# Kernel optimization log

Measured on AMD Instinct MI355X. Metric: run time of the kernel, lower is better.

Reference implementation:

```python
import jax, jax.numpy as jnp
import numpy as np

IN_SIZE = 256
HIDDEN = 512
T = 32768


def setup_inputs() -> dict:
    key = jax.random.key(0)
    ks = jax.random.split(key, 6)
    lim_ih = 1.0 / np.sqrt(HIDDEN)
    inp = {
        "input": jax.random.normal(ks[0], (T, IN_SIZE), dtype=jnp.float32),
        "init_hidden": jax.random.normal(ks[1], (HIDDEN,), dtype=jnp.float32),
        # eqx.nn.GRUCell parameters: weight_ih (3H, in), weight_hh (3H, H), bias (3H,), bias_n (H,)
        "weight_ih": jax.random.uniform(ks[2], (3 * HIDDEN, IN_SIZE), minval=-lim_ih, maxval=lim_ih, dtype=jnp.float32),
        "weight_hh": jax.random.uniform(ks[3], (3 * HIDDEN, HIDDEN), minval=-lim_ih, maxval=lim_ih, dtype=jnp.float32),
        "bias": jax.random.uniform(ks[4], (3 * HIDDEN,), minval=-lim_ih, maxval=lim_ih, dtype=jnp.float32),
        "bias_n": jax.random.uniform(ks[5], (HIDDEN,), minval=-lim_ih, maxval=lim_ih, dtype=jnp.float32),
    }
    return inp


def reference(input, init_hidden, weight_ih, weight_hh, bias, bias_n):
    H = init_hidden.shape[0]
    # Precompute all input-side gates in one big GEMM: [T, 3H]
    igates_all = input @ weight_ih.T + bias

    def step(h, ig):
        hg = weight_hh @ h  # [3H]
        ir, iz, inn = ig[:H], ig[H:2 * H], ig[2 * H:]
        hr, hz, hn = hg[:H], hg[H:2 * H], hg[2 * H:]
        reset = jax.nn.sigmoid(ir + hr)
        upd = jax.nn.sigmoid(iz + hz)
        new = jnp.tanh(inn + reset * (hn + bias_n))
        h_new = new + upd * (h - new)
        # rnn_out_o = atleast_2d(h_new) -> (1, H); [..., 0] -> (1,)
        return h_new, h_new[:1]

    _, out = jax.lax.scan(step, init_hidden, igates_all)
    return out  # [T, 1]
```

## Files before the change

kernel.cpp:

```cpp
#include <hip/hip_runtime.h>


#define T_STEPS    32768
#define INSZ       256
#define HSZ        512
#define NWG        32
#define TPB        1024
#define POLL_GUARD 16384

typedef unsigned long long u64;
typedef unsigned int u32;
typedef u32 u32x4 __attribute__((ext_vector_type(4)));
typedef float f32x4 __attribute__((ext_vector_type(4)));
typedef float f32x2 __attribute__((ext_vector_type(2)));

__device__ __forceinline__ float grp_reduce16(float v) {
  v += __shfl_xor(v, 1);
  v += __shfl_xor(v, 2);
  v += __shfl_xor(v, 4);
  v += __shfl_xor(v, 8);
  return v;
}

__device__ __forceinline__ int hpad(int k) { return k + 4 * (k >> 5); }

__device__ __forceinline__ void st16_sys(u64* p, u32x4 v) {
  asm volatile("global_store_dwordx4 %0, %1, off sc0 sc1" :: "v"(p), "v"(v) : "memory");
}

__device__ __forceinline__ void barrier_lds_only() {
  asm volatile("s_waitcnt lgkmcnt(0)\n\ts_barrier" ::: "memory");
}

__global__ void init_comm(u64* __restrict__ comm, const float* __restrict__ h0) {
  int jj = threadIdx.x;
  u32 bits = __float_as_uint(h0[jj]);
  comm[jj]       = (u64)bits;
  comm[HSZ + jj] = 0xFFFFFFFF00000000ull;
}

__launch_bounds__(256)
__global__ void igates_gemm(const float* __restrict__ input,
                            const float* __restrict__ w_ih,
                            const float* __restrict__ bias,
                            float* __restrict__ ig)
{
  const int t0 = blockIdx.x * 64;
  const int r0 = blockIdx.y * 64;
  const int tid = threadIdx.x;
  const int tx = tid & 15, ty = tid >> 4;
  __shared__ float As[64][68];
  __shared__ float Bs[64][68];
  float acc[4][4] = {};
  for (int kc = 0; kc < INSZ; kc += 64) {
    #pragma unroll
    for (int i = 0; i < 4; ++i) {
      const int rr = (tid >> 4) + 16 * i;
      f32x4 av = *(const f32x4*)&input[(size_t)(t0 + rr) * INSZ + kc + tx * 4];
      *(f32x4*)&As[rr][tx * 4] = av;
      f32x4 bv = *(const f32x4*)&w_ih[(size_t)(r0 + rr) * INSZ + kc + tx * 4];
      #pragma unroll
      for (int ci = 0; ci < 4; ++ci) Bs[tx * 4 + ci][rr] = bv[ci];
    }
    __syncthreads();
    #pragma unroll 16
    for (int kk = 0; kk < 64; ++kk) {
      float av[4], bv[4];
      #pragma unroll
      for (int a = 0; a < 4; ++a) av[a] = As[ty * 4 + a][kk];
      #pragma unroll
      for (int b = 0; b < 4; ++b) bv[b] = Bs[kk][tx * 4 + b];
      #pragma unroll
      for (int a = 0; a < 4; ++a)
        #pragma unroll
        for (int b = 0; b < 4; ++b) acc[a][b] += av[a] * bv[b];
    }
    __syncthreads();
  }
  #pragma unroll
  for (int a = 0; a < 4; ++a)
    #pragma unroll
    for (int b = 0; b < 4; ++b) {
      const int r = r0 + tx * 4 + b;
      ig[(size_t)(t0 + ty * 4 + a) * 1536 + r] = acc[a][b] + bias[r];
    }
}

__launch_bounds__(TPB, 1)
__global__ void gru_fast(const float* __restrict__ IG,
                         const float* __restrict__ init_hidden,
                         const float* __restrict__ w_hh,
                         const float* __restrict__ bias_n,
                         u64* __restrict__ comm,
                         float* __restrict__ out)
{
  const int tid = threadIdx.x;
  const int wg  = blockIdx.x;
  const int g   = tid >> 4;
  const int l   = tid & 15;
  const bool mv = (g < 48);
  const int R   = wg * 16 + (g & 15) + 512 * (g >> 4);

  f32x4 whh[8];
  if (mv) {
    const float* rp = w_hh + (size_t)R * HSZ + l * 32;
    #pragma unroll
    for (int c = 0; c < 8; ++c) whh[c] = *(const f32x4*)(rp + c * 4);
  }

  float hold = 0.f, bn = 0.f, ig_r = 0.f, ig_z = 0.f, ig_n = 0.f;
  if (tid < 16) {
    const int j = wg * 16 + tid;
    hold = init_hidden[j];
    bn   = bias_n[j];
    ig_r = IG[j];
    ig_z = IG[512 + j];
    ig_n = IG[1024 + j];
  }

  __shared__ float h_lds[2][HSZ + 4 * (HSZ >> 5)];
  __shared__ float gsum[48];

  const bool poller = (tid >= 768);
  const int  pt     = tid - 768;
  u32x4 pa, pb, pc, pd, win;

#define ISSUE(Rr) \
  asm volatile("global_load_dwordx4 %0, %1, off sc0 sc1" : "=&v"(Rr) : "v"(lp) : "memory")
#define CHECK(Rr) \
  asm volatile("s_waitcnt vmcnt(3)" : "+v"(Rr)); \
  __builtin_amdgcn_sched_barrier(0); \
  if ((Rr[1] == tt && Rr[3] == tt) || --guard == 0) { win = Rr; break; } \
  ISSUE(Rr)

  for (int t = 0; t < T_STEPS; ++t) {
    const int p  = t & 1;
    const u32 tt = (u32)t;

    if (poller) {
      const u64* lp = comm + (size_t)p * HSZ + 2 * pt;
      ISSUE(pa); ISSUE(pb); ISSUE(pc); ISSUE(pd);
      int guard = POLL_GUARD;
      win = pa;
      for (;;) {
        CHECK(pa);
        CHECK(pb);
        CHECK(pc);
        CHECK(pd);
      }
      f32x2 hv;
      hv[0] = __uint_as_float(win[0]);
      hv[1] = __uint_as_float(win[2]);
      *(f32x2*)&h_lds[p][hpad(2 * pt)] = hv;
    }
    barrier_lds_only();

    if (mv) {
      float a = 0.f;
      const float* hp = &h_lds[p][l * 36];
      #pragma unroll
      for (int c = 0; c < 8; ++c) {
        f32x4 hv4 = *(const f32x4*)(hp + c * 4);
        #pragma unroll
        for (int u = 0; u < 4; ++u) a += whh[c][u] * hv4[u];
      }
      a = grp_reduce16(a);
      if (l == 0) gsum[g] = a;
    }
    barrier_lds_only();

    if (tid < 16) {
      const int j = tid;
      const float hr = gsum[j], hz = gsum[16 + j], hn = gsum[32 + j];
      const float reset = __builtin_amdgcn_rcpf(1.0f + __expf(-(ig_r + hr)));
      const float upd   = __builtin_amdgcn_rcpf(1.0f + __expf(-(ig_z + hz)));
      const float e2    = __expf(2.0f * (ig_n + reset * (hn + bn)));
      const float newv  = 1.0f - 2.0f * __builtin_amdgcn_rcpf(1.0f + e2);
      const float hnew  = newv + upd * (hold - newv);
      hold = hnew;
      const float hpair = __shfl(hnew, tid + 1);
      if ((j & 1) == 0) {
        u64* nbuf = comm + (size_t)((t + 1) & 1) * HSZ;
        u32x4 pk;
        pk[0] = __float_as_uint(hnew);  pk[1] = (u32)(t + 1);
        pk[2] = __float_as_uint(hpair); pk[3] = (u32)(t + 1);
        st16_sys(&nbuf[wg * 16 + j], pk);
        if (wg == 0 && j == 0) out[t] = hnew;
      }
      const size_t bse = (size_t)((t + 1 < T_STEPS) ? (t + 1) : t) * 1536;
      const int jj = wg * 16 + tid;
      ig_r = IG[bse + jj];
      ig_z = IG[bse + 512 + jj];
      ig_n = IG[bse + 1024 + jj];
    }
  }
#undef ISSUE
#undef CHECK
  asm volatile("s_waitcnt vmcnt(0)" ::: "memory");
}

#define TPB_FB 1024
__device__ __forceinline__ int xpad(int k) { return k + ((k >> 4) << 2); }

__launch_bounds__(TPB_FB, 1)
__global__ void gru_persistent_fb(const float* __restrict__ input,
                                  const float* __restrict__ init_hidden,
                                  const float* __restrict__ w_ih,
                                  const float* __restrict__ w_hh,
                                  const float* __restrict__ bias,
                                  const float* __restrict__ bias_n,
                                  u64* __restrict__ comm,
                                  float* __restrict__ out)
{
  const int tid = threadIdx.x;
  const int wg  = blockIdx.x;
  const int g   = tid >> 4;
  const int l   = tid & 15;
  const bool mv = (g < 48);
  const int R   = wg * 16 + (g & 15) + 512 * (g >> 4);

  f32x4 whh[8];
  f32x4 wih[4];
  if (mv) {
    const float* rp = w_hh + (size_t)R * HSZ + l * 32;
    #pragma unroll
    for (int c = 0; c < 8; ++c) whh[c] = *(const f32x4*)(rp + c * 4);
    const float* rp2 = w_ih + (size_t)R * INSZ + l * 16;
    #pragma unroll
    for (int c = 0; c < 4; ++c) wih[c] = *(const f32x4*)(rp2 + c * 4);
  }
  float hold = 0.f, b_r = 0.f, b_z = 0.f, b_n = 0.f, bn = 0.f;
  if (tid < 16) {
    const int j = wg * 16 + tid;
    hold = init_hidden[j];
    b_r  = bias[j]; b_z = bias[j + 512]; b_n = bias[j + 1024];
    bn   = bias_n[j];
  }
  __shared__ float h_lds[2][HSZ + 4 * (HSZ >> 5)];
  __shared__ float gsum[48];
  __shared__ float isum[2][48];
  __shared__ float xstage[INSZ + (INSZ >> 4) * 4];

  if (tid >= 64 && tid < 128) {
    const int s = tid - 64;
    f32x4 v = *(const f32x4*)(input + s * 4);
    *(f32x4*)&xstage[xpad(s * 4)] = v;
  }
  __syncthreads();
  if (mv) {
    float a = 0.f;
    #pragma unroll
    for (int c = 0; c < 4; ++c) {
      f32x4 xv = *(const f32x4*)&xstage[20 * l + 4 * c];
      #pragma unroll
      for (int u = 0; u < 4; ++u) a += wih[c][u] * xv[u];
    }
    a = grp_reduce16(a);
    if (l == 0) isum[0][g] = a;
  }
  const bool poller = (tid >= 768);
  const int  pt     = tid - 768;
  u32x4 pa, pb, pc, pd, win;

#define ISSUE(Rr) \
  asm volatile("global_load_dwordx4 %0, %1, off sc0 sc1" : "=&v"(Rr) : "v"(lp) : "memory")
#define CHECK(Rr) \
  asm volatile("s_waitcnt vmcnt(3)" : "+v"(Rr)); \
  __builtin_amdgcn_sched_barrier(0); \
  if ((Rr[1] == tt && Rr[3] == tt) || --guard == 0) { win = Rr; break; } \
  ISSUE(Rr)

  for (int t = 0; t < T_STEPS; ++t) {
    const int p  = t & 1;
    const u32 tt = (u32)t;
    f32x4 xnew = {0.f, 0.f, 0.f, 0.f};
    if (tid >= 64 && tid < 128) {
      const int tn = (t + 1 < T_STEPS) ? (t + 1) : (T_STEPS - 1);
      xnew = *(const f32x4*)(input + (size_t)tn * INSZ + (tid - 64) * 4);
    }
    if (poller) {
      const u64* lp = comm + (size_t)p * HSZ + 2 * pt;
      ISSUE(pa); ISSUE(pb); ISSUE(pc); ISSUE(pd);
      int guard = POLL_GUARD;
      win = pa;
      for (;;) {
        CHECK(pa);
        CHECK(pb);
        CHECK(pc);
        CHECK(pd);
      }
      f32x2 hv;
      hv[0] = __uint_as_float(win[0]);
      hv[1] = __uint_as_float(win[2]);
      *(f32x2*)&h_lds[p][hpad(2 * pt)] = hv;
    }
    __syncthreads();
    if (mv) {
      float a = 0.f;
      const float* hp = &h_lds[p][l * 36];
      #pragma unroll
      for (int c = 0; c < 8; ++c) {
        f32x4 hv4 = *(const f32x4*)(hp + c * 4);
        #pragma unroll
        for (int u = 0; u < 4; ++u) a += whh[c][u] * hv4[u];
      }
      a = grp_reduce16(a);
      if (l == 0) gsum[g] = a;
    }
    if (tid >= 64 && tid < 128) *(f32x4*)&xstage[xpad((tid - 64) * 4)] = xnew;
    __syncthreads();
    if (tid < 16) {
      const int j = tid;
      const float hr = gsum[j], hz = gsum[16 + j], hn = gsum[32 + j];
      const float i_r = isum[p][j], i_z = isum[p][16 + j], i_n = isum[p][32 + j];
      const float reset = __builtin_amdgcn_rcpf(1.0f + __expf(-(i_r + b_r + hr)));
      const float upd   = __builtin_amdgcn_rcpf(1.0f + __expf(-(i_z + b_z + hz)));
      const float e2    = __expf(2.0f * (i_n + b_n + reset * (hn + bn)));
      const float newv  = 1.0f - 2.0f * __builtin_amdgcn_rcpf(1.0f + e2);
      const float hnew  = newv + upd * (hold - newv);
      hold = hnew;
      const float hpair = __shfl(hnew, tid + 1);
      if ((j & 1) == 0) {
        u64* nbuf = comm + (size_t)((t + 1) & 1) * HSZ;
        u32x4 pk;
        pk[0] = __float_as_uint(hnew);  pk[1] = (u32)(t + 1);
        pk[2] = __float_as_uint(hpair); pk[3] = (u32)(t + 1);
        st16_sys(&nbuf[wg * 16 + j], pk);
        if (wg == 0 && j == 0) out[t] = hnew;
      }
    }
    if (mv) {
      float a2 = 0.f;
      #pragma unroll
      for (int c = 0; c < 4; ++c) {
        f32x4 xv = *(const f32x4*)&xstage[20 * l + 4 * c];
        #pragma unroll
        for (int u = 0; u < 4; ++u) a2 += wih[c][u] * xv[u];
      }
      a2 = grp_reduce16(a2);
      if (l == 0) isum[(t + 1) & 1][g] = a2;
    }
  }
#undef ISSUE
#undef CHECK
}

extern "C" void kernel_launch(void* const* d_in, const int* in_sizes, int n_in,
                              void* d_out, int out_size, void* d_ws, size_t ws_size,
                              hipStream_t stream) {
  const float* input  = (const float*)d_in[0];
  const float* h0     = (const float*)d_in[1];
  const float* w_ih   = (const float*)d_in[2];
  const float* w_hh   = (const float*)d_in[3];
  const float* bias   = (const float*)d_in[4];
  const float* bias_n = (const float*)d_in[5];
  float* out = (float*)d_out;

  const size_t IG_BYTES = (size_t)T_STEPS * 1536 * sizeof(float);

  if (ws_size >= IG_BYTES + 16384) {
    float* ig  = (float*)d_ws;
    u64*  comm = (u64*)((char*)d_ws + IG_BYTES);
    hipLaunchKernelGGL(init_comm, dim3(1), dim3(HSZ), 0, stream, comm, h0);
    hipLaunchKernelGGL(igates_gemm, dim3(T_STEPS / 64, 1536 / 64), dim3(256),
                       0, stream, input, w_ih, bias, ig);
    hipLaunchKernelGGL(gru_fast, dim3(NWG), dim3(TPB), 0, stream,
                       ig, h0, w_hh, bias_n, comm, out);
  } else {
    u64* comm = (u64*)d_ws;
    hipLaunchKernelGGL(init_comm, dim3(1), dim3(HSZ), 0, stream, comm, h0);
    hipLaunchKernelGGL(gru_persistent_fb, dim3(NWG), dim3(TPB_FB), 0, stream,
                       input, h0, w_ih, w_hh, bias, bias_n, comm, out);
  }
}
```

Before: 51.80 ms.

## Map one hidden unit per wavefront across 64 workgroups, dropping gate-sum barrier

The recurrent kernel now runs on 64 workgroups. Each of the first 8 wavefronts owns one hidden unit and computes its r/z/n dot products, reduces them with shuffles and applies the GRU update inside the same wavefront. This removes the LDS gsum staging and the second workgroup barrier on every timestep, shortening the serial per-step critical path. The communication buffer becomes one duplicated 16-byte slot per hidden element, so 512 poller threads each poll a single element. That doubles the polling traffic and the number of participating workgroups that must synchronise through global memory.

```diff
diff --git a/kernel.cpp b/kernel.cpp
--- a/kernel.cpp
+++ b/kernel.cpp
@@ -4,7 +4,8 @@
 #define T_STEPS    32768
 #define INSZ       256
 #define HSZ        512
-#define NWG        32
+#define NWG        64
+#define RPW        8
 #define TPB        1024
 #define POLL_GUARD 16384
 
@@ -14,14 +15,6 @@
 typedef float f32x4 __attribute__((ext_vector_type(4)));
 typedef float f32x2 __attribute__((ext_vector_type(2)));
 
-__device__ __forceinline__ float grp_reduce16(float v) {
-  v += __shfl_xor(v, 1);
-  v += __shfl_xor(v, 2);
-  v += __shfl_xor(v, 4);
-  v += __shfl_xor(v, 8);
-  return v;
-}
-
 __device__ __forceinline__ int hpad(int k) { return k + 4 * (k >> 5); }
 
 __device__ __forceinline__ void st16_sys(u64* p, u32x4 v) {
@@ -34,9 +27,11 @@
 
 __global__ void init_comm(u64* __restrict__ comm, const float* __restrict__ h0) {
   int jj = threadIdx.x;
-  u32 bits = __float_as_uint(h0[jj]);
-  comm[jj]       = (u64)bits;
-  comm[HSZ + jj] = 0xFFFFFFFF00000000ull;
+  u64 v0 = (u64)__float_as_uint(h0[jj]);
+  comm[2 * jj]            = v0;
+  comm[2 * jj + 1]        = v0;
+  comm[1024 + 2 * jj]     = 0xFFFFFFFF00000000ull;
+  comm[1024 + 2 * jj + 1] = 0xFFFFFFFF00000000ull;
 }
 
 __launch_bounds__(256)
@@ -94,23 +89,25 @@
                          u64* __restrict__ comm,
                          float* __restrict__ out)
 {
-  const int tid = threadIdx.x;
-  const int wg  = blockIdx.x;
-  const int g   = tid >> 4;
-  const int l   = tid & 15;
-  const bool mv = (g < 48);
-  const int R   = wg * 16 + (g & 15) + 512 * (g >> 4);
+  const int tid  = threadIdx.x;
+  const int wg   = blockIdx.x;
+  const int wv   = tid >> 6;
+  const int lane = tid & 63;
+  const bool pol = (wv >= 8);
+  const int  pt  = (wv - 8) * 64 + lane;
+
+  const int j  = wg * RPW + wv;
+  const int q  = lane >> 4;
+  const int kl = lane & 15;
 
   f32x4 whh[8];
-  if (mv) {
-    const float* rp = w_hh + (size_t)R * HSZ + l * 32;
+  if (!pol && lane < 48) {
+    const float* rp = w_hh + (size_t)(j + 512 * q) * HSZ + kl * 32;
     #pragma unroll
     for (int c = 0; c < 8; ++c) whh[c] = *(const f32x4*)(rp + c * 4);
   }
-
   float hold = 0.f, bn = 0.f, ig_r = 0.f, ig_z = 0.f, ig_n = 0.f;
-  if (tid < 16) {
-    const int j = wg * 16 + tid;
+  if (!pol) {
     hold = init_hidden[j];
     bn   = bias_n[j];
     ig_r = IG[j];
@@ -119,10 +116,7 @@
   }
 
   __shared__ float h_lds[2][HSZ + 4 * (HSZ >> 5)];
-  __shared__ float gsum[48];
-
-  const bool poller = (tid >= 768);
-  const int  pt     = tid - 768;
+
   u32x4 pa, pb, pc, pd, win;
 
 #define ISSUE(Rr) \
@@ -137,8 +131,8 @@
     const int p  = t & 1;
     const u32 tt = (u32)t;
 
-    if (poller) {
-      const u64* lp = comm + (size_t)p * HSZ + 2 * pt;
+    if (pol) {
+      const u64* lp = comm + (size_t)p * 1024 + 2 * pt;
       ISSUE(pa); ISSUE(pb); ISSUE(pc); ISSUE(pd);
       int guard = POLL_GUARD;
       win = pa;
@@ -148,50 +142,44 @@
         CHECK(pc);
         CHECK(pd);
       }
-      f32x2 hv;
-      hv[0] = __uint_as_float(win[0]);
-      hv[1] = __uint_as_float(win[2]);
-      *(f32x2*)&h_lds[p][hpad(2 * pt)] = hv;
+      h_lds[p][hpad(pt)] = __uint_as_float(win[0]);
     }
     barrier_lds_only();
 
-    if (mv) {
+    if (!pol) {
       float a = 0.f;
-      const float* hp = &h_lds[p][l * 36];
+      const float* hp = &h_lds[p][kl * 36];
       #pragma unroll
       for (int c = 0; c < 8; ++c) {
         f32x4 hv4 = *(const f32x4*)(hp + c * 4);
         #pragma unroll
         for (int u = 0; u < 4; ++u) a += whh[c][u] * hv4[u];
       }
-      a = grp_reduce16(a);
-      if (l == 0) gsum[g] = a;
-    }
-    barrier_lds_only();
-
-    if (tid < 16) {
-      const int j = tid;
-      const float hr = gsum[j], hz = gsum[16 + j], hn = gsum[32 + j];
+      a += __shfl_xor(a, 1);
+      a += __shfl_xor(a, 2);
+      a += __shfl_xor(a, 4);
+      a += __shfl_xor(a, 8);
+      const float hr = __shfl(a, 0);
+      const float hz = __shfl(a, 16);
+      const float hn = __shfl(a, 32);
       const float reset = __builtin_amdgcn_rcpf(1.0f + __expf(-(ig_r + hr)));
       const float upd   = __builtin_amdgcn_rcpf(1.0f + __expf(-(ig_z + hz)));
       const float e2    = __expf(2.0f * (ig_n + reset * (hn + bn)));
       const float newv  = 1.0f - 2.0f * __builtin_amdgcn_rcpf(1.0f + e2);
       const float hnew  = newv + upd * (hold - newv);
       hold = hnew;
-      const float hpair = __shfl(hnew, tid + 1);
-      if ((j & 1) == 0) {
-        u64* nbuf = comm + (size_t)((t + 1) & 1) * HSZ;
+      if (lane == 0) {
+        u64* nbuf = comm + (size_t)((t + 1) & 1) * 1024;
         u32x4 pk;
         pk[0] = __float_as_uint(hnew);  pk[1] = (u32)(t + 1);
-        pk[2] = __float_as_uint(hpair); pk[3] = (u32)(t + 1);
-        st16_sys(&nbuf[wg * 16 + j], pk);
-        if (wg == 0 && j == 0) out[t] = hnew;
+        pk[2] = __float_as_uint(hnew);  pk[3] = (u32)(t + 1);
+        st16_sys(nbuf + 2 * j, pk);
+        if (wg == 0 && wv == 0) out[t] = hnew;
       }
       const size_t bse = (size_t)((t + 1 < T_STEPS) ? (t + 1) : t) * 1536;
-      const int jj = wg * 16 + tid;
-      ig_r = IG[bse + jj];
-      ig_z = IG[bse + 512 + jj];
-      ig_n = IG[bse + 1024 + jj];
+      ig_r = IG[bse + j];
+      ig_z = IG[bse + 512 + j];
+      ig_n = IG[bse + 1024 + j];
     }
   }
 #undef ISSUE
@@ -201,6 +189,13 @@
 
 #define TPB_FB 1024
 __device__ __forceinline__ int xpad(int k) { return k + ((k >> 4) << 2); }
+__device__ __forceinline__ float grp_reduce16(float v) {
+  v += __shfl_xor(v, 1);
+  v += __shfl_xor(v, 2);
+  v += __shfl_xor(v, 4);
+  v += __shfl_xor(v, 8);
+  return v;
+}
 
 __launch_bounds__(TPB_FB, 1)
 __global__ void gru_persistent_fb(const float* __restrict__ input,
@@ -358,7 +353,7 @@
 
   const size_t IG_BYTES = (size_t)T_STEPS * 1536 * sizeof(float);
 
-  if (ws_size >= IG_BYTES + 16384) {
+  if (ws_size >= IG_BYTES + 32768) {
     float* ig  = (float*)d_ws;
     u64*  comm = (u64*)((char*)d_ws + IG_BYTES);
     hipLaunchKernelGGL(init_comm, dim3(1), dim3(HSZ), 0, stream, comm, h0);
@@ -369,7 +364,7 @@
   } else {
     u64* comm = (u64*)d_ws;
     hipLaunchKernelGGL(init_comm, dim3(1), dim3(HSZ), 0, stream, comm, h0);
-    hipLaunchKernelGGL(gru_persistent_fb, dim3(NWG), dim3(TPB_FB), 0, stream,
+    hipLaunchKernelGGL(gru_persistent_fb, dim3(NWG / 2), dim3(TPB_FB), 0, stream,
                        input, h0, w_ih, w_hh, bias, bias_n, comm, out);
   }
 }
```

After: 100.7 ms. 94.3% more time.
